# Kernel optimization log

Measured on AMD Instinct MI355X. Metric: run time of the kernel, lower is better.

## Reference

```python
import jax, jax.numpy as jnp
import numpy as np

NP, NA = 60000, 30000          # paper / author node counts
EC, EW, EB = 300000, 150000, 150000
IN_F, HID, H, D, NCLS = 1024, 512, 4, 128, 153  # HID = H*D


def setup_inputs() -> dict:
    key = jax.random.key(0)
    ks = jax.random.split(key, 24)
    inp = {
        "x_paper": jax.random.normal(ks[0], (NP, IN_F), jnp.float32),
        "x_author": jax.random.normal(ks[1], (NA, IN_F), jnp.float32),
        "cites_src": jax.random.randint(ks[2], (EC,), 0, NP, jnp.int32),
        "cites_dst": jax.random.randint(ks[3], (EC,), 0, NP, jnp.int32),
        "writes_src": jax.random.randint(ks[4], (EW,), 0, NA, jnp.int32),
        "writes_dst": jax.random.randint(ks[5], (EW,), 0, NP, jnp.int32),
        "wb_src": jax.random.randint(ks[6], (EB,), 0, NP, jnp.int32),
        "wb_dst": jax.random.randint(ks[7], (EB,), 0, NA, jnp.int32),
        "W0": jax.random.normal(ks[8], (3, IN_F, HID), jnp.float32) * 0.02,
        "al0": jax.random.normal(ks[9], (3, H, D), jnp.float32) * 0.1,
        "ar0": jax.random.normal(ks[10], (3, H, D), jnp.float32) * 0.1,
        "W1": jax.random.normal(ks[11], (3, HID, HID), jnp.float32) * 0.03,
        "al1": jax.random.normal(ks[12], (3, H, D), jnp.float32) * 0.1,
        "ar1": jax.random.normal(ks[13], (3, H, D), jnp.float32) * 0.1,
        "W2": jax.random.normal(ks[14], (3, HID, HID), jnp.float32) * 0.03,
        "al2": jax.random.normal(ks[15], (3, H, D), jnp.float32) * 0.1,
        "ar2": jax.random.normal(ks[16], (3, H, D), jnp.float32) * 0.1,
        "linW": jax.random.normal(ks[17], (HID, NCLS), jnp.float32) * 0.02,
        "linb": jnp.zeros((NCLS,), jnp.float32),
    }
    return inp


def gat_conv(h_src, h_dst, src, dst, W, al, ar, n_dst):
    """DGL-style GATConv on one edge type (bipartite block, shared fc)."""
    zs = (h_src @ W).reshape(-1, H, D)            # (Ns,H,D)
    zd = (h_dst @ W).reshape(-1, H, D)            # (Nd,H,D)
    el = jnp.sum(zs * al, axis=-1)                # (Ns,H)
    er = jnp.sum(zd * ar, axis=-1)                # (Nd,H)
    e = jax.nn.leaky_relu(el[src] + er[dst], 0.2)  # (E,H)
    # edge softmax over incoming edges per destination node
    m = jax.ops.segment_max(e, dst, num_segments=n_dst)
    m = jnp.where(jnp.isfinite(m), m, 0.0)
    ee = jnp.exp(e - m[dst])
    s = jax.ops.segment_sum(ee, dst, num_segments=n_dst)
    a = ee / (s[dst] + 1e-9)                      # (E,H)
    # weighted message aggregation: (Nd,H,D)
    return jax.ops.segment_sum(a[:, :, None] * zs[src], dst, num_segments=n_dst)


def reference(x_paper, x_author, cites_src, cites_dst, writes_src, writes_dst,
              wb_src, wb_dst, W0, al0, ar0, W1, al1, ar1, W2, al2, ar2,
              linW, linb):
    def hetero_layer(hp, ha, W, al, ar, act):
        # HeteroGraphConv: sum-aggregate per destination node type
        op = (gat_conv(hp, hp, cites_src, cites_dst, W[0], al[0], ar[0], NP)
              + gat_conv(ha, hp, writes_src, writes_dst, W[1], al[1], ar[1], NP))
        oa = gat_conv(hp, ha, wb_src, wb_dst, W[2], al[2], ar[2], NA)
        op = op.reshape(NP, H * D)   # head-flatten as in forward()
        oa = oa.reshape(NA, H * D)
        if act:
            op, oa = jax.nn.relu(op), jax.nn.relu(oa)
        return op, oa

    hp, ha = x_paper, x_author
    hp, ha = hetero_layer(hp, ha, W0, al0, ar0, True)
    hp, ha = hetero_layer(hp, ha, W1, al1, ar1, True)
    hp, ha = hetero_layer(hp, ha, W2, al2, ar2, False)  # last layer: no activation
    return hp @ linW + linb
```

## Files before the change

kernel.cpp:

```cpp
#include <hip/hip_runtime.h>
#include <cstddef>
#include <cstdint>

static constexpr int NP = 60000, NA = 30000;
static constexpr int EC = 300000, EW = 150000, EB = 150000;
static constexpr int IN_F = 1024, HID = 512, H = 4, D = 128, NCLS = 153;
static constexpr int MPAD_P = 60160;
static constexpr int MPAD_A = 30208;

typedef __attribute__((ext_vector_type(8))) short short8;
typedef __attribute__((ext_vector_type(4))) float float4v;

__device__ __forceinline__ unsigned short f2bf(float f) {
    unsigned int u = __float_as_uint(f);
    unsigned int r = u + 0x7FFFu + ((u >> 16) & 1u);
    return (unsigned short)(r >> 16);
}
__device__ __forceinline__ float bf2f(unsigned short h) {
    return __uint_as_float(((unsigned int)h) << 16);
}

__device__ __forceinline__ void gll16(const unsigned short* g, unsigned short* l) {
    __builtin_amdgcn_global_load_lds(
        (const __attribute__((address_space(1))) unsigned int*)g,
        (__attribute__((address_space(3))) unsigned int*)l, 16, 0, 0);
}

__global__ void hist_kernel(const int* __restrict__ dst, int E, int* __restrict__ counts) {
    int e = blockIdx.x * 256 + threadIdx.x;
    if (e < E) atomicAdd(&counts[dst[e]], 1);
}

__global__ void exscan_kernel(const int* __restrict__ in, int* __restrict__ out, int n) {
    __shared__ int wsum[4];
    int t = threadIdx.x;
    int lane = t & 63, w = t >> 6;
    int carry = 0;
    const int CH = 256 * 8;
    for (int base = 0; base < n; base += CH) {
        int v[8], run[8];
        int i0 = base + t * 8;
        int tsum = 0;
#pragma unroll
        for (int j = 0; j < 8; ++j) {
            int i = i0 + j;
            v[j] = (i < n) ? in[i] : 0;
            tsum += v[j];
            run[j] = tsum;
        }
        int x = tsum;
#pragma unroll
        for (int off = 1; off < 64; off <<= 1) {
            int y = __shfl_up(x, off);
            if (lane >= off) x += y;
        }
        if (lane == 63) wsum[w] = x;
        __syncthreads();
        int wpre = 0;
        for (int ww = 0; ww < w; ++ww) wpre += wsum[ww];
        int chunktot = wsum[0] + wsum[1] + wsum[2] + wsum[3];
        int pre = carry + wpre + (x - tsum);
#pragma unroll
        for (int j = 0; j < 8; ++j) {
            int i = i0 + j;
            if (i < n) out[i] = pre + run[j] - v[j];
        }
        carry += chunktot;
        __syncthreads();
    }
    if (t == 0) out[n] = carry;
}

__global__ void fill_kernel(const int* __restrict__ src, const int* __restrict__ dst, int E,
                            int* __restrict__ cursor, int* __restrict__ col) {
    int e = blockIdx.x * 256 + threadIdx.x;
    if (e < E) {
        int pos = atomicAdd(&cursor[dst[e]], 1);
        col[pos] = src[e];
    }
}

__global__ void decomp4_kernel(const float4* __restrict__ x, ushort4* __restrict__ hi,
                               ushort4* __restrict__ lo, int M, int K, int Mpad) {
    size_t i4 = (size_t)blockIdx.x * 256 + threadIdx.x;
    size_t tot = ((size_t)Mpad * K) >> 2;
    if (i4 >= tot) return;
    size_t row = (i4 * 4) / (size_t)K;
    float4 v = make_float4(0.f, 0.f, 0.f, 0.f);
    if (row < (size_t)M) v = x[i4];
    ushort4 h, l;
    h.x = f2bf(v.x); h.y = f2bf(v.y); h.z = f2bf(v.z); h.w = f2bf(v.w);
    l.x = f2bf(v.x - bf2f(h.x)); l.y = f2bf(v.y - bf2f(h.y));
    l.z = f2bf(v.z - bf2f(h.z)); l.w = f2bf(v.w - bf2f(h.w));
    hi[i4] = h; lo[i4] = l;
}

__global__ void btprep_kernel(const float* __restrict__ W, unsigned short* __restrict__ hi,
                              unsigned short* __restrict__ lo, int K, int N, int Npad) {
    int i = blockIdx.x * 256 + threadIdx.x;
    if (i >= Npad * K) return;
    int n = i / K, k = i - n * K;
    float v = (n < N) ? W[(size_t)k * N + n] : 0.f;
    unsigned short h = f2bf(v);
    hi[i] = h;
    lo[i] = f2bf(v - bf2f(h));
}

__global__ __launch_bounds__(512, 2) void gemm_8ph(
    const unsigned short* __restrict__ Ahi, const unsigned short* __restrict__ Alo,
    const unsigned short* __restrict__ Bhi, const unsigned short* __restrict__ Blo,
    const float* __restrict__ bias, float* __restrict__ C,
    int M, int K, int Nstore, int ldc) {
    extern __shared__ unsigned short lds[];
    const int tid = threadIdx.x;
    const int lane = tid & 63;
    const int w = tid >> 6;
    const int wr = w >> 2, wc = w & 3;
    const int bm = blockIdx.y * 256, bn = blockIdx.x * 256;

    const int st_row = w * 16 + (lane >> 2);
    const int st_sc = (((lane & 3) ^ ((lane >> 3) & 3)) << 3);
    const size_t aoff0 = (size_t)(bm + st_row) * K + st_sc;
    const size_t aoff1 = aoff0 + (size_t)128 * K;
    const size_t boff0 = (size_t)(bn + st_row) * K + st_sc;
    const size_t boff1 = boff0 + (size_t)128 * K;
    const int ldsA = w * 512;
    const int ldsB = 8192 + w * 512;

    const int arow = wr * 128 + (lane & 15);
    const int brow = wc * 64 + (lane & 15);
    const int rq = ((((lane >> 4) & 3) ^ ((lane >> 1) & 3)) << 3);
    const int aRead = arow * 32 + rq;
    const int bRead = 8192 + brow * 32 + rq;

    float4v acc[8][4];
    float4v zf = {0.f, 0.f, 0.f, 0.f};
#pragma unroll
    for (int i = 0; i < 8; ++i)
#pragma unroll
        for (int j = 0; j < 4; ++j) acc[i][j] = zf;

    auto STAGE_ALL = [&](unsigned rr, const unsigned short* As, const unsigned short* Bs, int kc) {
        unsigned short* sb = &lds[rr * 16384u];
        gll16(As + aoff0 + kc, sb + ldsA);
        gll16(As + aoff1 + kc, sb + ldsA + 4096);
        gll16(Bs + boff0 + kc, sb + ldsB);
        gll16(Bs + boff1 + kc, sb + ldsB + 4096);
    };

#define WAITV(n) asm volatile("s_waitcnt vmcnt(" #n ")" ::: "memory")
#define BARF()                                 \
    do {                                       \
        asm volatile("" ::: "memory");         \
        __builtin_amdgcn_s_barrier();          \
        asm volatile("" ::: "memory");         \
    } while (0)

#define TILE(RR, ASRC, BSRC, KN, DOSTAGE, WAITSTMT)                                   \
    do {                                                                              \
        const unsigned short* sb = &lds[(RR) * 16384u];                               \
        unsigned short* db = &lds[(((RR) + 3u) & 3u) * 16384u];                       \
        short8 fa[4], fb[4];                                                          \
        _Pragma("unroll") for (int i = 0; i < 4; ++i)                                 \
            fa[i] = *(const short8*)&sb[aRead + i * 512];                             \
        _Pragma("unroll") for (int j = 0; j < 4; ++j)                                 \
            fb[j] = *(const short8*)&sb[bRead + j * 512];                             \
        if (DOSTAGE) {                                                                \
            gll16(ASRC + aoff0 + (KN), db + ldsA);                                    \
            gll16(ASRC + aoff1 + (KN), db + ldsA + 4096);                             \
        }                                                                             \
        BARF();                                                                       \
        __builtin_amdgcn_s_setprio(1);                                                \
        _Pragma("unroll") for (int i = 0; i < 4; ++i)                                 \
            _Pragma("unroll") for (int j = 0; j < 4; ++j)                             \
                acc[i][j] = __builtin_amdgcn_mfma_f32_16x16x32_bf16(fa[i], fb[j], acc[i][j], 0, 0, 0); \
        __builtin_amdgcn_s_setprio(0);                                                \
        BARF();                                                                       \
        short8 fa2[4];                                                                \
        _Pragma("unroll") for (int i = 0; i < 4; ++i)                                 \
            fa2[i] = *(const short8*)&sb[aRead + (i + 4) * 512];                      \
        if (DOSTAGE) {                                                                \
            gll16(BSRC + boff0 + (KN), db + ldsB);                                    \
            gll16(BSRC + boff1 + (KN), db + ldsB + 4096);                             \
        }                                                                             \
        BARF();                                                                       \
        __builtin_amdgcn_s_setprio(1);                                                \
        _Pragma("unroll") for (int i = 0; i < 4; ++i)                                 \
            _Pragma("unroll") for (int j = 0; j < 4; ++j)                             \
                acc[i + 4][j] = __builtin_amdgcn_mfma_f32_16x16x32_bf16(fa2[i], fb[j], acc[i + 4][j], 0, 0, 0); \
        __builtin_amdgcn_s_setprio(0);                                                \
        WAITSTMT;                                                                     \
        BARF();                                                                       \
    } while (0)

    STAGE_ALL(0, Ahi, Bhi, 0);
    STAGE_ALL(1, Alo, Bhi, 0);
    STAGE_ALL(2, Ahi, Blo, 0);
    WAITV(8);
    BARF();

    unsigned rg = 0;
    const int nK = K >> 5;
#pragma unroll 1
    for (int c = 0; c < nK - 1; ++c) {
        const int kn = (c + 1) << 5;
        TILE(rg, Ahi, Bhi, kn, 1, WAITV(8));
        rg = (rg + 1) & 3;
        TILE(rg, Alo, Bhi, kn, 1, WAITV(8));
        rg = (rg + 1) & 3;
        TILE(rg, Ahi, Blo, kn, 1, WAITV(8));
        rg = (rg + 1) & 3;
    }
    TILE(rg, Ahi, Bhi, 0, 0, WAITV(4));
    rg = (rg + 1) & 3;
    TILE(rg, Alo, Bhi, 0, 0, WAITV(0));
    rg = (rg + 1) & 3;
    TILE(rg, Ahi, Blo, 0, 0, (void)0);
#undef TILE
#undef WAITV
#undef BARF

    const int col0 = bn + wc * 64 + (lane & 15);
    const int row0 = bm + wr * 128 + ((lane >> 4) << 2);
#pragma unroll
    for (int i = 0; i < 8; ++i) {
#pragma unroll
        for (int j = 0; j < 4; ++j) {
            int col = col0 + j * 16;
            if (col >= Nstore) continue;
            float badd = bias ? bias[col] : 0.f;
            int rowb = row0 + i * 16;
#pragma unroll
            for (int k = 0; k < 4; ++k) {
                int row = rowb + k;
                if (row < M) C[(size_t)row * ldc + col] = acc[i][j][k] + badd;
            }
        }
    }
}

__global__ __launch_bounds__(256) void eler_kernel(
    const float* __restrict__ z, const float* __restrict__ al, const float* __restrict__ ar,
    float* __restrict__ el, float* __restrict__ er, int M) {
    int row = blockIdx.x * 4 + (threadIdx.x >> 6);
    int lane = threadIdx.x & 63;
    if (row >= M) return;
    const float4* zr = (const float4*)(z + (size_t)row * 512 + lane * 8);
    float4 z0 = zr[0], z1 = zr[1];
    const float4* alp = (const float4*)(al + lane * 8);
    float4 a0 = alp[0], a1 = alp[1];
    float s = z0.x * a0.x + z0.y * a0.y + z0.z * a0.z + z0.w * a0.w
            + z1.x * a1.x + z1.y * a1.y + z1.z * a1.z + z1.w * a1.w;
    s += __shfl_xor(s, 8); s += __shfl_xor(s, 4); s += __shfl_xor(s, 2); s += __shfl_xor(s, 1);
    int h = lane >> 4;
    if ((lane & 15) == 0) el[(size_t)row * 4 + h] = s;
    if (er) {
        const float4* arp = (const float4*)(ar + lane * 8);
        float4 b0 = arp[0], b1 = arp[1];
        float t = z0.x * b0.x + z0.y * b0.y + z0.z * b0.z + z0.w * b0.w
                + z1.x * b1.x + z1.y * b1.y + z1.z * b1.z + z1.w * b1.w;
        t += __shfl_xor(t, 8); t += __shfl_xor(t, 4); t += __shfl_xor(t, 2); t += __shfl_xor(t, 1);
        if ((lane & 15) == 0) er[(size_t)row * 4 + h] = t;
    }
}

__global__ void fold_kernel(const float* __restrict__ W, const float* __restrict__ ar,
                            float* __restrict__ v, int K) {
    int i = blockIdx.x * 256 + threadIdx.x;
    if (i >= K * 4) return;
    int k = i >> 2, h = i & 3;
    const float* wr = W + (size_t)k * 512 + h * 128;
    const float* a = ar + h * 128;
    float s = 0.f;
#pragma unroll 4
    for (int d = 0; d < 128; ++d) s += wr[d] * a[d];
    v[i] = s;
}

__global__ __launch_bounds__(256) void skinny_kernel(
    const float* __restrict__ h, const float* __restrict__ v,
    float* __restrict__ er, int M, int K) {
    __shared__ float vs[4096];
    for (int i = threadIdx.x; i < K * 4; i += 256) vs[i] = v[i];
    __syncthreads();
    int row = blockIdx.x * 4 + (threadIdx.x >> 6);
    int lane = threadIdx.x & 63;
    if (row >= M) return;
    const float* hr = h + (size_t)row * K;
    float a0 = 0, a1 = 0, a2 = 0, a3 = 0;
    for (int k = lane; k < K; k += 64) {
        float x = hr[k];
        float4 vv = *(const float4*)&vs[k * 4];
        a0 += x * vv.x; a1 += x * vv.y; a2 += x * vv.z; a3 += x * vv.w;
    }
#pragma unroll
    for (int off = 32; off; off >>= 1) {
        a0 += __shfl_xor(a0, off); a1 += __shfl_xor(a1, off);
        a2 += __shfl_xor(a2, off); a3 += __shfl_xor(a3, off);
    }
    if (lane == 0) *(float4*)&er[(size_t)row * 4] = make_float4(a0, a1, a2, a3);
}

__global__ __launch_bounds__(256) void agg_fused(
    const int* __restrict__ rp1, const int* __restrict__ col1, const float* __restrict__ z1,
    const float* __restrict__ el1, const float* __restrict__ er1,
    const int* __restrict__ rp2, const int* __restrict__ col2, const float* __restrict__ z2,
    const float* __restrict__ el2, const float* __restrict__ er2,
    float* __restrict__ out, unsigned short* __restrict__ hi, unsigned short* __restrict__ lo,
    int N, int do_relu) {
    int j = blockIdx.x * 4 + (threadIdx.x >> 6);
    int lane = threadIdx.x & 63;
    if (j >= N) return;
    int h = lane >> 4;
    float4 acc0 = make_float4(0, 0, 0, 0), acc1 = make_float4(0, 0, 0, 0);

    {
        int e0 = rp1[j], e1 = rp1[j + 1];
        float erh = er1[(size_t)j * 4 + h];
        float m = -INFINITY, s = 0.f;
        for (int e = e0; e < e1; ++e) {
            float x = el1[(size_t)col1[e] * 4 + h] + erh;
            x = (x >= 0.f) ? x : 0.2f * x;
            float mn = fmaxf(m, x);
            s = s * expf(m - mn) + expf(x - mn);
            m = mn;
        }
        float inv = 1.0f / (s + 1e-9f);
        for (int e = e0; e < e1; ++e) {
            int src = col1[e];
            float x = el1[(size_t)src * 4 + h] + erh;
            x = (x >= 0.f) ? x : 0.2f * x;
            float wgt = expf(x - m) * inv;
            const float4* zr = (const float4*)(z1 + (size_t)src * 512 + lane * 8);
            float4 za = zr[0], zb = zr[1];
            acc0.x += wgt * za.x; acc0.y += wgt * za.y; acc0.z += wgt * za.z; acc0.w += wgt * za.w;
            acc1.x += wgt * zb.x; acc1.y += wgt * zb.y; acc1.z += wgt * zb.z; acc1.w += wgt * zb.w;
        }
    }
    if (rp2) {
        int e0 = rp2[j], e1 = rp2[j + 1];
        float erh = er2[(size_t)j * 4 + h];
        float m = -INFINITY, s = 0.f;
        for (int e = e0; e < e1; ++e) {
            float x = el2[(size_t)col2[e] * 4 + h] + erh;
            x = (x >= 0.f) ? x : 0.2f * x;
            float mn = fmaxf(m, x);
            s = s * expf(m - mn) + expf(x - mn);
            m = mn;
        }
        float inv = 1.0f / (s + 1e-9f);
        for (int e = e0; e < e1; ++e) {
            int src = col2[e];
            float x = el2[(size_t)src * 4 + h] + erh;
            x = (x >= 0.f) ? x : 0.2f * x;
            float wgt = expf(x - m) * inv;
            const float4* zr = (const float4*)(z2 + (size_t)src * 512 + lane * 8);
            float4 za = zr[0], zb = zr[1];
            acc0.x += wgt * za.x; acc0.y += wgt * za.y; acc0.z += wgt * za.z; acc0.w += wgt * za.w;
            acc1.x += wgt * zb.x; acc1.y += wgt * zb.y; acc1.z += wgt * zb.z; acc1.w += wgt * zb.w;
        }
    }
    if (do_relu) {
        acc0.x = fmaxf(acc0.x, 0.f); acc0.y = fmaxf(acc0.y, 0.f);
        acc0.z = fmaxf(acc0.z, 0.f); acc0.w = fmaxf(acc0.w, 0.f);
        acc1.x = fmaxf(acc1.x, 0.f); acc1.y = fmaxf(acc1.y, 0.f);
        acc1.w = fmaxf(acc1.w, 0.f); acc1.z = fmaxf(acc1.z, 0.f);
    }
    float* op = out + (size_t)j * 512 + lane * 8;
    *(float4*)op = acc0;
    *(float4*)(op + 4) = acc1;
    if (hi) {
        size_t base = (size_t)j * 512 + lane * 8;
        ushort4 h0, h1, l0, l1;
        h0.x = f2bf(acc0.x); h0.y = f2bf(acc0.y); h0.z = f2bf(acc0.z); h0.w = f2bf(acc0.w);
        h1.x = f2bf(acc1.x); h1.y = f2bf(acc1.y); h1.z = f2bf(acc1.z); h1.w = f2bf(acc1.w);
        l0.x = f2bf(acc0.x - bf2f(h0.x)); l0.y = f2bf(acc0.y - bf2f(h0.y));
        l0.z = f2bf(acc0.z - bf2f(h0.z)); l0.w = f2bf(acc0.w - bf2f(h0.w));
        l1.x = f2bf(acc1.x - bf2f(h1.x)); l1.y = f2bf(acc1.y - bf2f(h1.y));
        l1.z = f2bf(acc1.z - bf2f(h1.z)); l1.w = f2bf(acc1.w - bf2f(h1.w));
        *(ushort4*)(hi + base) = h0;
        *(ushort4*)(hi + base + 4) = h1;
        *(ushort4*)(lo + base) = l0;
        *(ushort4*)(lo + base + 4) = l1;
    }
}

extern "C" void kernel_launch(void* const* d_in, const int* in_sizes, int n_in,
                              void* d_out, int out_size, void* d_ws, size_t ws_size,
                              hipStream_t stream) {
    const float* x_paper = (const float*)d_in[0];
    const float* x_author = (const float*)d_in[1];
    const int* cites_src = (const int*)d_in[2];
    const int* cites_dst = (const int*)d_in[3];
    const int* writes_src = (const int*)d_in[4];
    const int* writes_dst = (const int*)d_in[5];
    const int* wb_src = (const int*)d_in[6];
    const int* wb_dst = (const int*)d_in[7];
    const float* W0 = (const float*)d_in[8];
    const float* al0 = (const float*)d_in[9];
    const float* ar0 = (const float*)d_in[10];
    const float* W1 = (const float*)d_in[11];
    const float* al1 = (const float*)d_in[12];
    const float* ar1 = (const float*)d_in[13];
    const float* W2 = (const float*)d_in[14];
    const float* al2 = (const float*)d_in[15];
    const float* ar2 = (const float*)d_in[16];
    const float* linW = (const float*)d_in[17];
    const float* linb = (const float*)d_in[18];
    float* out = (float*)d_out;

    (void)hipFuncSetAttribute((const void*)gemm_8ph,
                              hipFuncAttributeMaxDynamicSharedMemorySize, 131072);

    char* p = (char*)d_ws;
    auto alloc = [&](size_t n) { char* r = p; p += (n + 255) & ~(size_t)255; return r; };

    float* hpA = (float*)alloc((size_t)NP * 512 * 4);
    float* hpB = (float*)alloc((size_t)NP * 512 * 4);
    float* haA = (float*)alloc((size_t)NA * 512 * 4);
    float* haB = (float*)alloc((size_t)NA * 512 * 4);
    float* zbuf = (float*)alloc((size_t)NP * 512 * 4);
    float* elA = (float*)alloc((size_t)NP * 16);
    float* erA = (float*)alloc((size_t)NP * 16);
    float* elB = (float*)alloc((size_t)NP * 16);
    float* erB = (float*)alloc((size_t)NP * 16);
    float* vfold = (float*)alloc(4096 * 4);
    int* rp_c = (int*)alloc((NP + 1) * 4);
    int* col_c = (int*)alloc((size_t)EC * 4);
    int* rp_w = (int*)alloc((NP + 1) * 4);
    int* col_w = (int*)alloc((size_t)EW * 4);
    int* rp_b = (int*)alloc((NA + 1) * 4);
    int* col_b = (int*)alloc((size_t)EB * 4);
    int* cursor = (int*)alloc((NP + 1) * 4);
    int* counts = (int*)alloc((size_t)NP * 4);

    unsigned short* AhiP = (unsigned short*)alloc((size_t)MPAD_P * 1024 * 2);
    unsigned short* AloP = (unsigned short*)alloc((size_t)MPAD_P * 1024 * 2);
    unsigned short* AhiA = (unsigned short*)alloc((size_t)MPAD_A * 1024 * 2);
    unsigned short* AloA = (unsigned short*)alloc((size_t)MPAD_A * 1024 * 2);
    const int Ks[3] = {IN_F, HID, HID};
    unsigned short *bthi[3][3], *btlo[3][3];
    for (int l = 0; l < 3; ++l)
        for (int t = 0; t < 3; ++t) {
            bthi[l][t] = (unsigned short*)alloc((size_t)512 * Ks[l] * 2);
            btlo[l][t] = (unsigned short*)alloc((size_t)512 * Ks[l] * 2);
        }
    unsigned short* btLhi = (unsigned short*)alloc((size_t)256 * 512 * 2);
    unsigned short* btLlo = (unsigned short*)alloc((size_t)256 * 512 * 2);
    (void)ws_size;

    struct EdgeT { const int* src; const int* dst; int E; int n; int* rp; int* col; };
    EdgeT ets[3] = {
        {cites_src, cites_dst, EC, NP, rp_c, col_c},
        {writes_src, writes_dst, EW, NP, rp_w, col_w},
        {wb_src, wb_dst, EB, NA, rp_b, col_b},
    };
    for (int t = 0; t < 3; ++t) {
        hipMemsetAsync(counts, 0, (size_t)ets[t].n * 4, stream);
        hist_kernel<<<(ets[t].E + 255) / 256, 256, 0, stream>>>(ets[t].dst, ets[t].E, counts);
        exscan_kernel<<<1, 256, 0, stream>>>(counts, ets[t].rp, ets[t].n);
        hipMemcpyAsync(cursor, ets[t].rp, (size_t)ets[t].n * 4, hipMemcpyDeviceToDevice, stream);
        fill_kernel<<<(ets[t].E + 255) / 256, 256, 0, stream>>>(ets[t].src, ets[t].dst, ets[t].E, cursor, ets[t].col);
    }

    const float* Wl[3] = {W0, W1, W2};
    const float* alL[3] = {al0, al1, al2};
    const float* arL[3] = {ar0, ar1, ar2};

    for (int l = 0; l < 3; ++l) {
        int K = Ks[l];
        for (int t = 0; t < 3; ++t)
            btprep_kernel<<<(512 * K + 255) / 256, 256, 0, stream>>>(
                Wl[l] + (size_t)t * K * 512, bthi[l][t], btlo[l][t], K, 512, 512);
    }
    btprep_kernel<<<(256 * 512 + 255) / 256, 256, 0, stream>>>(linW, btLhi, btLlo, 512, NCLS, 256);

    decomp4_kernel<<<((size_t)MPAD_P * 1024 / 4 + 255) / 256, 256, 0, stream>>>(
        (const float4*)x_paper, (ushort4*)AhiP, (ushort4*)AloP, NP, 1024, MPAD_P);
    decomp4_kernel<<<((size_t)MPAD_A * 1024 / 4 + 255) / 256, 256, 0, stream>>>(
        (const float4*)x_author, (ushort4*)AhiA, (ushort4*)AloA, NA, 1024, MPAD_A);

    auto gemm = [&](const unsigned short* Ah, const unsigned short* Al,
                    const unsigned short* Bh, const unsigned short* Bl,
                    const float* bias, float* C, int M, int Mpad, int K, int gx,
                    int Nstore, int ldc) {
        dim3 g(gx, Mpad / 256);
        gemm_8ph<<<g, 512, 131072, stream>>>(Ah, Al, Bh, Bl, bias, C, M, K, Nstore, ldc);
    };

    const float* hp = x_paper;
    const float* ha = x_author;
    for (int l = 0; l < 3; ++l) {
        int K = Ks[l];
        float* hp_n = (l & 1) ? hpB : hpA;
        float* ha_n = (l & 1) ? haB : haA;
        float* zbuf_w = ha_n;
        const float* W = Wl[l];
        const float* al = alL[l];
        const float* ar = arL[l];
        size_t wstride = (size_t)K * 512;
        int relu = (l < 2) ? 1 : 0;

        gemm(AhiP, AloP, bthi[l][0], btlo[l][0], nullptr, zbuf, NP, MPAD_P, K, 2, 512, 512);
        gemm(AhiA, AloA, bthi[l][1], btlo[l][1], nullptr, zbuf_w, NA, MPAD_A, K, 2, 512, 512);
        eler_kernel<<<(NP + 3) / 4, 256, 0, stream>>>(zbuf, al, ar, elA, erA, NP);
        eler_kernel<<<(NA + 3) / 4, 256, 0, stream>>>(zbuf_w, al + 512, nullptr, elB, nullptr, NA);
        fold_kernel<<<(K * 4 + 255) / 256, 256, 0, stream>>>(W + wstride, ar + 512, vfold, K);
        skinny_kernel<<<(NP + 3) / 4, 256, 0, stream>>>(hp, vfold, erB, NP, K);
        agg_fused<<<(NP + 3) / 4, 256, 0, stream>>>(
            rp_c, col_c, zbuf, elA, erA,
            rp_w, col_w, zbuf_w, elB, erB,
            hp_n, nullptr, nullptr, NP, relu);
        gemm(AhiP, AloP, bthi[l][2], btlo[l][2], nullptr, zbuf, NP, MPAD_P, K, 2, 512, 512);
        decomp4_kernel<<<((size_t)MPAD_P * 512 / 4 + 255) / 256, 256, 0, stream>>>(
            (const float4*)hp_n, (ushort4*)AhiP, (ushort4*)AloP, NP, 512, MPAD_P);
        eler_kernel<<<(NP + 3) / 4, 256, 0, stream>>>(zbuf, al + 1024, nullptr, elA, nullptr, NP);
        fold_kernel<<<(K * 4 + 255) / 256, 256, 0, stream>>>(W + 2 * wstride, ar + 1024, vfold, K);
        skinny_kernel<<<(NA + 3) / 4, 256, 0, stream>>>(ha, vfold, erA, NA, K);
        agg_fused<<<(NA + 3) / 4, 256, 0, stream>>>(
            rp_b, col_b, zbuf, elA, erA,
            nullptr, nullptr, nullptr, nullptr, nullptr,
            ha_n, (l < 2) ? AhiA : nullptr, (l < 2) ? AloA : nullptr, NA, relu);
        hp = hp_n;
        ha = ha_n;
    }
    gemm(AhiP, AloP, btLhi, btLlo, linb, out, NP, MPAD_P, 512, 1, NCLS, NCLS);
}
```

Before: 3.318 ms.

## Restructure split-bf16 GEMM pipeline to reuse hi fragments across three products

The 3-pass split-bf16 GEMM used to stage each of the three products (Ahi*Bhi, Alo*Bhi, Ahi*Blo) as its own tile through a 4-slot LDS ring, reloading A and B tiles separately for each. It now stages all four hi/lo A and B tiles for a K-chunk into two double-buffered slot pairs and runs the three products from registers that stay loaded: Bhi fragments are reused for the Alo product and Ahi fragments for the Blo product. This removes redundant global-to-LDS loads and LDS reads, and cuts the work per K-step to six phases from eight. The cost is more live fragment registers and a shallower prefetch depth (two buffers instead of three ahead), which could hurt latency hiding or occupancy.

```diff
diff --git a/kernel.cpp b/kernel.cpp
--- a/kernel.cpp
+++ b/kernel.cpp
@@ -106,7 +106,7 @@
     lo[i] = f2bf(v - bf2f(h));
 }
 
-__global__ __launch_bounds__(512, 2) void gemm_8ph(
+__global__ __launch_bounds__(512, 2) void gemm_6ph(
     const unsigned short* __restrict__ Ahi, const unsigned short* __restrict__ Alo,
     const unsigned short* __restrict__ Bhi, const unsigned short* __restrict__ Blo,
     const float* __restrict__ bias, float* __restrict__ C,
@@ -124,8 +124,8 @@
     const size_t aoff1 = aoff0 + (size_t)128 * K;
     const size_t boff0 = (size_t)(bn + st_row) * K + st_sc;
     const size_t boff1 = boff0 + (size_t)128 * K;
-    const int ldsA = w * 512;
-    const int ldsB = 8192 + w * 512;
+    const int ldsAo = w * 512;
+    const int ldsBo = 8192 + w * 512;
 
     const int arow = wr * 128 + (lane & 15);
     const int brow = wc * 64 + (lane & 15);
@@ -139,14 +139,6 @@
     for (int i = 0; i < 8; ++i)
 #pragma unroll
         for (int j = 0; j < 4; ++j) acc[i][j] = zf;
-
-    auto STAGE_ALL = [&](unsigned rr, const unsigned short* As, const unsigned short* Bs, int kc) {
-        unsigned short* sb = &lds[rr * 16384u];
-        gll16(As + aoff0 + kc, sb + ldsA);
-        gll16(As + aoff1 + kc, sb + ldsA + 4096);
-        gll16(Bs + boff0 + kc, sb + ldsB);
-        gll16(Bs + boff1 + kc, sb + ldsB + 4096);
-    };
 
 #define WAITV(n) asm volatile("s_waitcnt vmcnt(" #n ")" ::: "memory")
 #define BARF()                                 \
@@ -155,48 +147,86 @@
         __builtin_amdgcn_s_barrier();          \
         asm volatile("" ::: "memory");         \
     } while (0)
-
-#define TILE(RR, ASRC, BSRC, KN, DOSTAGE, WAITSTMT)                                   \
+#define PRIO1 __builtin_amdgcn_s_setprio(1)
+#define PRIO0 __builtin_amdgcn_s_setprio(0)
+#define MF(a, b, c) __builtin_amdgcn_mfma_f32_16x16x32_bf16(a, b, c, 0, 0, 0)
+
+#define CHUNK(RG, DOSTAGE, KN, W2STMT, W6STMT)                                        \
     do {                                                                              \
-        const unsigned short* sb = &lds[(RR) * 16384u];                               \
-        unsigned short* db = &lds[(((RR) + 3u) & 3u) * 16384u];                       \
-        short8 fa[4], fb[4];                                                          \
-        _Pragma("unroll") for (int i = 0; i < 4; ++i)                                 \
-            fa[i] = *(const short8*)&sb[aRead + i * 512];                             \
+        const unsigned short* sA = &lds[(RG) * 16384u];             \
+        const unsigned short* sB = &lds[((RG) + 1u) * 16384u];      \
+        unsigned short* dA = &lds[((RG) ^ 2u) * 16384u];                              \
+        unsigned short* dB = &lds[(((RG) ^ 2u) + 1u) * 16384u];                       \
+        short8 fahi[8], falo[8], fbhi[4], fblo[4];                                    \
+                                                                  \
+        _Pragma("unroll") for (int i = 0; i < 4; ++i)                                 \
+            fahi[i] = *(const short8*)&sA[aRead + i * 512];                           \
         _Pragma("unroll") for (int j = 0; j < 4; ++j)                                 \
-            fb[j] = *(const short8*)&sb[bRead + j * 512];                             \
+            fbhi[j] = *(const short8*)&sA[bRead + j * 512];                           \
         if (DOSTAGE) {                                                                \
-            gll16(ASRC + aoff0 + (KN), db + ldsA);                                    \
-            gll16(ASRC + aoff1 + (KN), db + ldsA + 4096);                             \
+            gll16(Ahi + aoff0 + (KN), dA + ldsAo);                                    \
+            gll16(Ahi + aoff1 + (KN), dA + ldsAo + 4096);                             \
         }                                                                             \
-        BARF();                                                                       \
-        __builtin_amdgcn_s_setprio(1);                                                \
+        BARF(); PRIO1;                                                                \
         _Pragma("unroll") for (int i = 0; i < 4; ++i)                                 \
             _Pragma("unroll") for (int j = 0; j < 4; ++j)                             \
-                acc[i][j] = __builtin_amdgcn_mfma_f32_16x16x32_bf16(fa[i], fb[j], acc[i][j], 0, 0, 0); \
-        __builtin_amdgcn_s_setprio(0);                                                \
-        BARF();                                                                       \
-        short8 fa2[4];                                                                \
-        _Pragma("unroll") for (int i = 0; i < 4; ++i)                                 \
-            fa2[i] = *(const short8*)&sb[aRead + (i + 4) * 512];                      \
+                acc[i][j] = MF(fahi[i], fbhi[j], acc[i][j]);                          \
+        PRIO0; BARF();                                                                \
+                                                                  \
+        _Pragma("unroll") for (int i = 0; i < 4; ++i)                                 \
+            fahi[i + 4] = *(const short8*)&sA[aRead + (i + 4) * 512];                 \
         if (DOSTAGE) {                                                                \
-            gll16(BSRC + boff0 + (KN), db + ldsB);                                    \
-            gll16(BSRC + boff1 + (KN), db + ldsB + 4096);                             \
+            gll16(Bhi + boff0 + (KN), dA + ldsBo);                                    \
+            gll16(Bhi + boff1 + (KN), dA + ldsBo + 4096);                             \
         }                                                                             \
-        BARF();                                                                       \
-        __builtin_amdgcn_s_setprio(1);                                                \
+        BARF(); PRIO1;                                                                \
         _Pragma("unroll") for (int i = 0; i < 4; ++i)                                 \
             _Pragma("unroll") for (int j = 0; j < 4; ++j)                             \
-                acc[i + 4][j] = __builtin_amdgcn_mfma_f32_16x16x32_bf16(fa2[i], fb[j], acc[i + 4][j], 0, 0, 0); \
-        __builtin_amdgcn_s_setprio(0);                                                \
-        WAITSTMT;                                                                     \
-        BARF();                                                                       \
+                acc[i + 4][j] = MF(fahi[i + 4], fbhi[j], acc[i + 4][j]);              \
+        PRIO0; W2STMT; BARF();                                                        \
+                                                                  \
+        _Pragma("unroll") for (int i = 0; i < 4; ++i)                                 \
+            falo[i] = *(const short8*)&sB[aRead + i * 512];                           \
+        if (DOSTAGE) {                                                                \
+            gll16(Alo + aoff0 + (KN), dB + ldsAo);                                    \
+            gll16(Alo + aoff1 + (KN), dB + ldsAo + 4096);                             \
+        }                                                                             \
+        BARF(); PRIO1;                                                                \
+        _Pragma("unroll") for (int i = 0; i < 4; ++i)                                 \
+            _Pragma("unroll") for (int j = 0; j < 4; ++j)                             \
+                acc[i][j] = MF(falo[i], fbhi[j], acc[i][j]);                          \
+        PRIO0; BARF();                                                                \
+                                                                  \
+        _Pragma("unroll") for (int i = 0; i < 4; ++i)                                 \
+            falo[i + 4] = *(const short8*)&sB[aRead + (i + 4) * 512];                 \
+        if (DOSTAGE) {                                                                \
+            gll16(Blo + boff0 + (KN), dB + ldsBo);                                    \
+            gll16(Blo + boff1 + (KN), dB + ldsBo + 4096);                             \
+        }                                                                             \
+        BARF(); PRIO1;                                                                \
+        _Pragma("unroll") for (int i = 0; i < 4; ++i)                                 \
+            _Pragma("unroll") for (int j = 0; j < 4; ++j)                             \
+                acc[i + 4][j] = MF(falo[i + 4], fbhi[j], acc[i + 4][j]);              \
+        PRIO0; BARF();                                                                \
+                                      \
+        _Pragma("unroll") for (int j = 0; j < 4; ++j)                                 \
+            fblo[j] = *(const short8*)&sB[bRead + j * 512];                           \
+        BARF(); PRIO1;                                                                \
+        _Pragma("unroll") for (int i = 0; i < 8; ++i)                                 \
+            _Pragma("unroll") for (int j = 0; j < 4; ++j)                             \
+                acc[i][j] = MF(fahi[i], fblo[j], acc[i][j]);                          \
+        PRIO0; W6STMT; BARF();                                                        \
     } while (0)
 
-    STAGE_ALL(0, Ahi, Bhi, 0);
-    STAGE_ALL(1, Alo, Bhi, 0);
-    STAGE_ALL(2, Ahi, Blo, 0);
-    WAITV(8);
+    gll16(Ahi + aoff0, &lds[0] + ldsAo);
+    gll16(Ahi + aoff1, &lds[0] + ldsAo + 4096);
+    gll16(Bhi + boff0, &lds[0] + ldsBo);
+    gll16(Bhi + boff1, &lds[0] + ldsBo + 4096);
+    gll16(Alo + aoff0, &lds[16384] + ldsAo);
+    gll16(Alo + aoff1, &lds[16384] + ldsAo + 4096);
+    gll16(Blo + boff0, &lds[16384] + ldsBo);
+    gll16(Blo + boff1, &lds[16384] + ldsBo + 4096);
+    WAITV(4);
     BARF();
 
     unsigned rg = 0;
@@ -204,19 +234,14 @@
 #pragma unroll 1
     for (int c = 0; c < nK - 1; ++c) {
         const int kn = (c + 1) << 5;
-        TILE(rg, Ahi, Bhi, kn, 1, WAITV(8));
-        rg = (rg + 1) & 3;
-        TILE(rg, Alo, Bhi, kn, 1, WAITV(8));
-        rg = (rg + 1) & 3;
-        TILE(rg, Ahi, Blo, kn, 1, WAITV(8));
-        rg = (rg + 1) & 3;
-    }
-    TILE(rg, Ahi, Bhi, 0, 0, WAITV(4));
-    rg = (rg + 1) & 3;
-    TILE(rg, Alo, Bhi, 0, 0, WAITV(0));
-    rg = (rg + 1) & 3;
-    TILE(rg, Ahi, Blo, 0, 0, (void)0);
-#undef TILE
+        CHUNK(rg, 1, kn, WAITV(4), WAITV(4));
+        rg ^= 2;
+    }
+    CHUNK(rg, 0, 0, WAITV(0), (void)0);
+#undef CHUNK
+#undef MF
+#undef PRIO1
+#undef PRIO0
 #undef WAITV
 #undef BARF
 
@@ -364,7 +389,7 @@
         acc0.x = fmaxf(acc0.x, 0.f); acc0.y = fmaxf(acc0.y, 0.f);
         acc0.z = fmaxf(acc0.z, 0.f); acc0.w = fmaxf(acc0.w, 0.f);
         acc1.x = fmaxf(acc1.x, 0.f); acc1.y = fmaxf(acc1.y, 0.f);
-        acc1.w = fmaxf(acc1.w, 0.f); acc1.z = fmaxf(acc1.z, 0.f);
+        acc1.z = fmaxf(acc1.z, 0.f); acc1.w = fmaxf(acc1.w, 0.f);
     }
     float* op = out + (size_t)j * 512 + lane * 8;
     *(float4*)op = acc0;
@@ -409,7 +434,7 @@
     const float* linb = (const float*)d_in[18];
     float* out = (float*)d_out;
 
-    (void)hipFuncSetAttribute((const void*)gemm_8ph,
+    (void)hipFuncSetAttribute((const void*)gemm_6ph,
                               hipFuncAttributeMaxDynamicSharedMemorySize, 131072);
 
     char* p = (char*)d_ws;
@@ -485,7 +510,7 @@
                     const float* bias, float* C, int M, int Mpad, int K, int gx,
                     int Nstore, int ldc) {
         dim3 g(gx, Mpad / 256);
-        gemm_8ph<<<g, 512, 131072, stream>>>(Ah, Al, Bh, Bl, bias, C, M, K, Nstore, ldc);
+        gemm_6ph<<<g, 512, 131072, stream>>>(Ah, Al, Bh, Bl, bias, C, M, K, Nstore, ldc);
     };
 
     const float* hp = x_paper;
```

Measured after the change: 3.216 ms. 3.1% less time.
